# Performance work log

Hardware: AMD Instinct MI355X
Metric: run time of the kernel (lower is better)

Reference implementation:

```python
import jax, jax.numpy as jnp
import numpy as np
import math

D, S, B = 64, 2048, 16  # head_dim, seq_len, batch (inputs stored as [D, S, B])


def setup_inputs() -> dict:
    key = jax.random.key(0)
    kq, kk, kv = jax.random.split(key, 3)
    return {
        "Q": jax.random.normal(kq, (D, S, B), dtype=jnp.float32),
        "K": jax.random.normal(kk, (D, S, B), dtype=jnp.float32),
        "V": jax.random.normal(kv, (D, S, B), dtype=jnp.float32),
        "d_k": S,
    }


def reference(Q, K, V, d_k):
    # transpose(0, 2): [D, S, B] -> [B, S, D]
    q = jnp.transpose(Q, (2, 1, 0))
    k = jnp.transpose(K, (2, 1, 0))
    v = jnp.transpose(V, (2, 1, 0))
    # bmm(_Q, K_T) * 1/sqrt(d_k): [B, S, S]
    scores = jnp.einsum("bsd,btd->bst", q, k) * (1.0 / math.sqrt(d_k))
    # original does view(-1, d_k) + Softmax over dim=1; with d_k == last dim
    # this is a softmax over the key axis. Dropout is identity in eval mode.
    probs = jax.nn.softmax(scores, axis=-1)
    out = jnp.einsum("bst,btd->bsd", probs, v)  # [B, S, D]
    # transpose(0, 2) back: [D, S, B]
    return jnp.transpose(out, (2, 1, 0))
```

## Files before the change

### kernel.cpp

```cpp
#include <hip/hip_runtime.h>
#include <hip/hip_bf16.h>

#define D_ 64
#define S_ 2048
#define B_ 16
#define QT 64
#define KVT 128

typedef short short8 __attribute__((ext_vector_type(8)));
typedef float floatx4 __attribute__((ext_vector_type(4)));
typedef unsigned uint2v __attribute__((ext_vector_type(2)));
typedef unsigned uint4v __attribute__((ext_vector_type(4)));

#define SC2 (1.4426950408889634f / 45.254833995939045f)

__device__ __forceinline__ unsigned short f2bf(float f) {
  unsigned u = __builtin_bit_cast(unsigned, f);
  u += 0x7fffu + ((u >> 16) & 1u);
  return (unsigned short)(u >> 16);
}

__device__ __forceinline__ unsigned pk2(float a, float b) {
  __hip_bfloat162 h = __float22bfloat162_rn(float2{a, b});
  unsigned r;
  __builtin_memcpy(&r, &h, sizeof(r));
  return r;
}

__global__ __launch_bounds__(256) void pack_all(const float* __restrict__ Q,
                                                const float* __restrict__ K,
                                                const float* __restrict__ V,
                                                unsigned short* __restrict__ Qp,
                                                unsigned short* __restrict__ Kp,
                                                unsigned short* __restrict__ Vt) {
  __shared__ __align__(16) unsigned short tile[256][72];
  const int t = threadIdx.x;
  const int bid = blockIdx.x;
  if (bid < 256) {
    const bool isK = bid >= 128;
    const float* src = isK ? K : Q;
    unsigned short* dst = isK ? Kp : Qp;
    const float scale = isK ? SC2 : 1.0f;
    const int rb = bid & 127;
    const int s0 = rb * 16;
#pragma unroll
    for (int i = 0; i < 16; i++) {
      int j = i * 256 + t;
      int d = j >> 6;
      int sb4 = (j & 63) * 4;
      const float4 v = *(const float4*)(src + (size_t)d * (S_ * B_) + s0 * B_ + sb4);
      float vv[4] = {v.x, v.y, v.z, v.w};
#pragma unroll
      for (int k = 0; k < 4; k++) {
        int sb = sb4 + k;
        tile[(sb & 15) * 16 + (sb >> 4)][d] = f2bf(vv[k] * scale);
      }
    }
    __syncthreads();
#pragma unroll
    for (int i = 0; i < 8; i++) {
      int j = i * 256 + t;
      int r = j >> 3, c = j & 7;
      int b = r >> 4, si = r & 15;
      uint4 v = *(const uint4*)(&tile[r][c * 8]);
      *(uint4*)(dst + (((size_t)(b * 128 + rb)) << 10) + ((c >> 2) << 9) +
                (((c & 3) * 16 + si) << 3)) = v;
    }
  } else {
    const int vb = bid - 256;
    const int s0 = (vb & 31) * 64;
    const int d0 = (vb >> 5) * 16;
    const int dblk = vb >> 5;
#pragma unroll
    for (int i = 0; i < 16; i++) {
      int j = i * 256 + t;
      int dd = j >> 8;
      int sb4 = (j & 255) * 4;
      const float4 v = *(const float4*)(V + (size_t)(d0 + dd) * (S_ * B_) + s0 * B_ + sb4);
      float vv[4] = {v.x, v.y, v.z, v.w};
#pragma unroll
      for (int k = 0; k < 4; k++) {
        int sb = sb4 + k;
        tile[(sb & 15) * 16 + dd][sb >> 4] = f2bf(vv[k]);
      }
    }
    __syncthreads();
#pragma unroll
    for (int i = 0; i < 8; i++) {
      int j = i * 256 + t;
      int b = j >> 7;
      int c32r = (j >> 6) & 1;
      int l = j & 63, g = l >> 4, ln = l & 15;
      const unsigned short* row = &tile[b * 16 + ln][c32r * 32];
      uint2 u0 = *(const uint2*)(row + g * 4);
      uint2 u1 = *(const uint2*)(row + 16 + g * 4);
      int c32 = (s0 >> 5) + c32r;
      uint4 o = make_uint4(u0.x, u0.y, u1.x, u1.y);
      *(uint4*)(Vt + (((size_t)(b * 64 + c32) * 4 + dblk) << 9) + l * 8) = o;
    }
  }
}

__global__ __launch_bounds__(256, 2) void attn(const unsigned short* __restrict__ Qp,
                                               const unsigned short* __restrict__ Kp,
                                               const unsigned short* __restrict__ Vt,
                                               float* __restrict__ Ot) {
  __shared__ __align__(16) char smem_[69632 + 1024];
  float* red = (float*)smem_;
  float* lred = (float*)(smem_ + 69632);

  const int tid = threadIdx.x;
  const int w = tid >> 6, l = tid & 63, g = l >> 4, ln = l & 15;
  const int b = blockIdx.x & 15;
  const int q0 = (int)(blockIdx.x >> 4) * QT;

  const unsigned short* Qb = Qp + ((size_t)b << 17);
  const unsigned short* Kb = Kp + ((size_t)b << 17);
  const unsigned short* Vb = Vt + ((size_t)b << 17);

  const unsigned short* Qw = Qb + (((size_t)(q0 >> 4)) << 10) + l * 8;
  const unsigned short* Kw = Kb + w * 2048 + l * 8;
  const unsigned short* Vw = Vb + w * 2048 + l * 8;

  short8 qf[4][2];
#pragma unroll
  for (int nf = 0; nf < 4; nf++)
#pragma unroll
    for (int ks = 0; ks < 2; ks++)
      qf[nf][ks] = *(const short8*)(Qw + nf * 1024 + ks * 512);

  short8 kf[2][2];
#pragma unroll
  for (int mf = 0; mf < 2; mf++)
#pragma unroll
    for (int ks = 0; ks < 2; ks++)
      kf[mf][ks] = *(const short8*)(Kw + mf * 1024 + ks * 512);

  short8 vf[4];
#pragma unroll
  for (int mfd = 0; mfd < 4; mfd++)
    vf[mfd] = *(const short8*)(Vw + mfd * 512);

  const short8 ones8 = {(short)0x3F80, (short)0x3F80, (short)0x3F80, (short)0x3F80,
                        (short)0x3F80, (short)0x3F80, (short)0x3F80, (short)0x3F80};
  const floatx4 ZERO = {0.f, 0.f, 0.f, 0.f};
  floatx4 oacc[4][4];
  floatx4 dacc[4];
#pragma unroll
  for (int mfd = 0; mfd < 4; mfd++)
#pragma unroll
    for (int nf = 0; nf < 4; nf++) oacc[mfd][nf] = ZERO;
#pragma unroll
  for (int nf = 0; nf < 4; nf++) dacc[nf] = ZERO;

  for (int t = 0; t < 16; t++) {
    const int tn = ((t + 1) & 15) * 8192;

    floatx4 sacc[2][4];
    __builtin_amdgcn_s_setprio(1);
#pragma unroll
    for (int mf = 0; mf < 2; mf++)
#pragma unroll
      for (int nf = 0; nf < 4; nf++)
        sacc[mf][nf] = __builtin_amdgcn_mfma_f32_16x16x32_bf16(kf[mf][0], qf[nf][0],
                                                               ZERO, 0, 0, 0);
#pragma unroll
    for (int mf = 0; mf < 2; mf++)
#pragma unroll
      for (int nf = 0; nf < 4; nf++)
        sacc[mf][nf] = __builtin_amdgcn_mfma_f32_16x16x32_bf16(kf[mf][1], qf[nf][1],
                                                               sacc[mf][nf], 0, 0, 0);
    __builtin_amdgcn_s_setprio(0);

#pragma unroll
    for (int mf = 0; mf < 2; mf++)
#pragma unroll
      for (int ks = 0; ks < 2; ks++)
        kf[mf][ks] = *(const short8*)(Kw + tn + mf * 1024 + ks * 512);

    short8 pbf[4];
#pragma unroll
    for (int nf = 0; nf < 4; nf++) {
      unsigned p00 = pk2(__builtin_amdgcn_exp2f(sacc[0][nf][0]),
                         __builtin_amdgcn_exp2f(sacc[0][nf][1]));
      unsigned p01 = pk2(__builtin_amdgcn_exp2f(sacc[0][nf][2]),
                         __builtin_amdgcn_exp2f(sacc[0][nf][3]));
      unsigned p10 = pk2(__builtin_amdgcn_exp2f(sacc[1][nf][0]),
                         __builtin_amdgcn_exp2f(sacc[1][nf][1]));
      unsigned p11 = pk2(__builtin_amdgcn_exp2f(sacc[1][nf][2]),
                         __builtin_amdgcn_exp2f(sacc[1][nf][3]));
      pbf[nf] = __builtin_bit_cast(short8, (uint4v){p00, p01, p10, p11});
    }

    __builtin_amdgcn_s_setprio(1);
#pragma unroll
    for (int nf = 0; nf < 4; nf++)
      dacc[nf] = __builtin_amdgcn_mfma_f32_16x16x32_bf16(ones8, pbf[nf], dacc[nf], 0, 0, 0);

#pragma unroll
    for (int mfd = 0; mfd < 4; mfd++)
#pragma unroll
      for (int nf = 0; nf < 4; nf++)
        oacc[mfd][nf] = __builtin_amdgcn_mfma_f32_16x16x32_bf16(vf[mfd], pbf[nf],
                                                                oacc[mfd][nf], 0, 0, 0);
    __builtin_amdgcn_s_setprio(0);

#pragma unroll
    for (int mfd = 0; mfd < 4; mfd++)
      vf[mfd] = *(const short8*)(Vw + tn + mfd * 512);
  }

  if (g == 0) {
#pragma unroll
    for (int nf = 0; nf < 4; nf++) lred[w * 64 + nf * 16 + ln] = dacc[nf][0];
  }
#pragma unroll
  for (int mfd = 0; mfd < 4; mfd++)
#pragma unroll
    for (int nf = 0; nf < 4; nf++)
      *(floatx4*)(&red[w * 4352 + (nf * 16 + ln) * 68 + mfd * 16 + g * 4]) = oacc[mfd][nf];
  __syncthreads();

  const int q = l;
  const float denom = lred[q] + lred[64 + q] + lred[128 + q] + lred[192 + q];
  const float linv = 1.0f / denom;
#pragma unroll
  for (int i = 0; i < 4; i++) {
    floatx4 s = (floatx4){0.f, 0.f, 0.f, 0.f};
#pragma unroll
    for (int w2 = 0; w2 < 4; w2++)
      s += *(const floatx4*)(&red[w2 * 4352 + q * 68 + w * 16 + i * 4]);
    s *= linv;
#pragma unroll
    for (int r = 0; r < 4; r++)
      Ot[(size_t)(b * D_ + w * 16 + i * 4 + r) * S_ + q0 + q] = s[r];
  }
}

__global__ __launch_bounds__(256) void unpack_o(const float* __restrict__ Ot,
                                                float* __restrict__ out) {
  const int d0 = (int)(blockIdx.x & 7) * 8;
  const int s0 = (int)(blockIdx.x >> 3) * 64;
  __shared__ float u[8 * 1024];
  const int t = threadIdx.x;
#pragma unroll
  for (int i = 0; i < 8; i++) {
    int j = i * 256 + t;
    int d = j >> 8, bb = (j >> 4) & 15, c = j & 15;
    float4 v = *(const float4*)(Ot + (size_t)(bb * D_ + d0 + d) * S_ + s0 + c * 4);
    float vv[4] = {v.x, v.y, v.z, v.w};
#pragma unroll
    for (int k = 0; k < 4; k++) {
      int si = c * 4 + k;
      int W = si * 16 + bb;
      int Wp = W ^ ((si & 15) << 2);
      u[d * 1024 + Wp] = vv[k];
    }
  }
  __syncthreads();
#pragma unroll
  for (int i = 0; i < 8; i++) {
    int j = i * 256 + t;
    int d = j >> 8, c2 = j & 255;
    int G = c2 ^ ((c2 >> 2) & 15);
    float4 v = *(const float4*)(&u[d * 1024 + G * 4]);
    *(float4*)(out + (size_t)(d0 + d) * (S_ * B_) + s0 * B_ + c2 * 4) = v;
  }
}

extern "C" void kernel_launch(void* const* d_in, const int* in_sizes, int n_in,
                              void* d_out, int out_size, void* d_ws, size_t ws_size,
                              hipStream_t stream) {
  const float* Q = (const float*)d_in[0];
  const float* K = (const float*)d_in[1];
  const float* V = (const float*)d_in[2];
  float* out = (float*)d_out;
  char* ws = (char*)d_ws;
  unsigned short* Qp = (unsigned short*)(ws);
  unsigned short* Kp = (unsigned short*)(ws + (4u << 20));
  unsigned short* Vt = (unsigned short*)(ws + (8u << 20));
  float* Ot = (float*)(ws + (12u << 20));

  hipLaunchKernelGGL(pack_all, dim3(384), dim3(256), 0, stream, Q, K, V, Qp, Kp, Vt);
  hipLaunchKernelGGL(attn, dim3(512), dim3(256), 0, stream, Qp, Kp, Vt, Ot);
  hipLaunchKernelGGL(unpack_o, dim3(256), dim3(256), 0, stream, Ot, out);
}
```

Baseline: 100.8 us.

## Split query tile across wave halves and compute softmax denominators with VALU adds

The attention block grows from 256 to 512 threads. Each group of four waves now handles half the 64-query tile, so per-wave accumulators shrink and per-CU wave occupancy may rise. The row-sum MFMA against a ones vector is replaced by scalar adds of the exponentials, and the cross-wave reduction now runs in two phases through a much smaller shared buffer. Each wave still streams the same K/V, so the extra waves add more K/V load traffic per block and an extra barrier.

```diff
diff --git a/kernel.cpp b/kernel.cpp
--- a/kernel.cpp
+++ b/kernel.cpp
@@ -9,7 +9,6 @@
 
 typedef short short8 __attribute__((ext_vector_type(8)));
 typedef float floatx4 __attribute__((ext_vector_type(4)));
-typedef unsigned uint2v __attribute__((ext_vector_type(2)));
 typedef unsigned uint4v __attribute__((ext_vector_type(4)));
 
 #define SC2 (1.4426950408889634f / 45.254833995939045f)
@@ -101,16 +100,16 @@
   }
 }
 
-__global__ __launch_bounds__(256, 2) void attn(const unsigned short* __restrict__ Qp,
+__global__ __launch_bounds__(512, 4) void attn(const unsigned short* __restrict__ Qp,
                                                const unsigned short* __restrict__ Kp,
                                                const unsigned short* __restrict__ Vt,
                                                float* __restrict__ Ot) {
-  __shared__ __align__(16) char smem_[69632 + 1024];
-  float* red = (float*)smem_;
-  float* lred = (float*)(smem_ + 69632);
+  __shared__ __align__(16) float red[2][2][32][68];
+  __shared__ float lred[2][4][4][32];
 
   const int tid = threadIdx.x;
   const int w = tid >> 6, l = tid & 63, g = l >> 4, ln = l & 15;
+  const int qh = w >> 2, ksw = w & 3;
   const int b = blockIdx.x & 15;
   const int q0 = (int)(blockIdx.x >> 4) * QT;
 
@@ -118,13 +117,13 @@
   const unsigned short* Kb = Kp + ((size_t)b << 17);
   const unsigned short* Vb = Vt + ((size_t)b << 17);
 
-  const unsigned short* Qw = Qb + (((size_t)(q0 >> 4)) << 10) + l * 8;
-  const unsigned short* Kw = Kb + w * 2048 + l * 8;
-  const unsigned short* Vw = Vb + w * 2048 + l * 8;
-
-  short8 qf[4][2];
-#pragma unroll
-  for (int nf = 0; nf < 4; nf++)
+  const unsigned short* Qw = Qb + (((size_t)((q0 >> 4) + qh * 2)) << 10) + l * 8;
+  const unsigned short* Kw = Kb + ksw * 2048 + l * 8;
+  const unsigned short* Vw = Vb + ksw * 2048 + l * 8;
+
+  short8 qf[2][2];
+#pragma unroll
+  for (int nf = 0; nf < 2; nf++)
 #pragma unroll
     for (int ks = 0; ks < 2; ks++)
       qf[nf][ks] = *(const short8*)(Qw + nf * 1024 + ks * 512);
@@ -141,33 +140,29 @@
   for (int mfd = 0; mfd < 4; mfd++)
     vf[mfd] = *(const short8*)(Vw + mfd * 512);
 
-  const short8 ones8 = {(short)0x3F80, (short)0x3F80, (short)0x3F80, (short)0x3F80,
-                        (short)0x3F80, (short)0x3F80, (short)0x3F80, (short)0x3F80};
   const floatx4 ZERO = {0.f, 0.f, 0.f, 0.f};
-  floatx4 oacc[4][4];
-  floatx4 dacc[4];
+  floatx4 oacc[4][2];
+  float dacc[2] = {0.f, 0.f};
 #pragma unroll
   for (int mfd = 0; mfd < 4; mfd++)
 #pragma unroll
-    for (int nf = 0; nf < 4; nf++) oacc[mfd][nf] = ZERO;
-#pragma unroll
-  for (int nf = 0; nf < 4; nf++) dacc[nf] = ZERO;
+    for (int nf = 0; nf < 2; nf++) oacc[mfd][nf] = ZERO;
 
   for (int t = 0; t < 16; t++) {
     const int tn = ((t + 1) & 15) * 8192;
 
-    floatx4 sacc[2][4];
+    floatx4 sacc[2][2];
     __builtin_amdgcn_s_setprio(1);
 #pragma unroll
     for (int mf = 0; mf < 2; mf++)
 #pragma unroll
-      for (int nf = 0; nf < 4; nf++)
+      for (int nf = 0; nf < 2; nf++)
         sacc[mf][nf] = __builtin_amdgcn_mfma_f32_16x16x32_bf16(kf[mf][0], qf[nf][0],
                                                                ZERO, 0, 0, 0);
 #pragma unroll
     for (int mf = 0; mf < 2; mf++)
 #pragma unroll
-      for (int nf = 0; nf < 4; nf++)
+      for (int nf = 0; nf < 2; nf++)
         sacc[mf][nf] = __builtin_amdgcn_mfma_f32_16x16x32_bf16(kf[mf][1], qf[nf][1],
                                                                sacc[mf][nf], 0, 0, 0);
     __builtin_amdgcn_s_setprio(0);
@@ -178,29 +173,28 @@
       for (int ks = 0; ks < 2; ks++)
         kf[mf][ks] = *(const short8*)(Kw + tn + mf * 1024 + ks * 512);
 
-    short8 pbf[4];
-#pragma unroll
-    for (int nf = 0; nf < 4; nf++) {
-      unsigned p00 = pk2(__builtin_amdgcn_exp2f(sacc[0][nf][0]),
-                         __builtin_amdgcn_exp2f(sacc[0][nf][1]));
-      unsigned p01 = pk2(__builtin_amdgcn_exp2f(sacc[0][nf][2]),
-                         __builtin_amdgcn_exp2f(sacc[0][nf][3]));
-      unsigned p10 = pk2(__builtin_amdgcn_exp2f(sacc[1][nf][0]),
-                         __builtin_amdgcn_exp2f(sacc[1][nf][1]));
-      unsigned p11 = pk2(__builtin_amdgcn_exp2f(sacc[1][nf][2]),
-                         __builtin_amdgcn_exp2f(sacc[1][nf][3]));
+    short8 pbf[2];
+#pragma unroll
+    for (int nf = 0; nf < 2; nf++) {
+      float e0 = __builtin_amdgcn_exp2f(sacc[0][nf][0]);
+      float e1 = __builtin_amdgcn_exp2f(sacc[0][nf][1]);
+      float e2 = __builtin_amdgcn_exp2f(sacc[0][nf][2]);
+      float e3 = __builtin_amdgcn_exp2f(sacc[0][nf][3]);
+      float e4 = __builtin_amdgcn_exp2f(sacc[1][nf][0]);
+      float e5 = __builtin_amdgcn_exp2f(sacc[1][nf][1]);
+      float e6 = __builtin_amdgcn_exp2f(sacc[1][nf][2]);
+      float e7 = __builtin_amdgcn_exp2f(sacc[1][nf][3]);
+      unsigned p00 = pk2(e0, e1), p01 = pk2(e2, e3);
+      unsigned p10 = pk2(e4, e5), p11 = pk2(e6, e7);
       pbf[nf] = __builtin_bit_cast(short8, (uint4v){p00, p01, p10, p11});
+      dacc[nf] += ((e0 + e1) + (e2 + e3)) + ((e4 + e5) + (e6 + e7));
     }
 
     __builtin_amdgcn_s_setprio(1);
 #pragma unroll
-    for (int nf = 0; nf < 4; nf++)
-      dacc[nf] = __builtin_amdgcn_mfma_f32_16x16x32_bf16(ones8, pbf[nf], dacc[nf], 0, 0, 0);
-
-#pragma unroll
-    for (int mfd = 0; mfd < 4; mfd++)
-#pragma unroll
-      for (int nf = 0; nf < 4; nf++)
+    for (int mfd = 0; mfd < 4; mfd++)
+#pragma unroll
+      for (int nf = 0; nf < 2; nf++)
         oacc[mfd][nf] = __builtin_amdgcn_mfma_f32_16x16x32_bf16(vf[mfd], pbf[nf],
                                                                 oacc[mfd][nf], 0, 0, 0);
     __builtin_amdgcn_s_setprio(0);
@@ -210,30 +204,47 @@
       vf[mfd] = *(const short8*)(Vw + tn + mfd * 512);
   }
 
-  if (g == 0) {
-#pragma unroll
-    for (int nf = 0; nf < 4; nf++) lred[w * 64 + nf * 16 + ln] = dacc[nf][0];
-  }
-#pragma unroll
-  for (int mfd = 0; mfd < 4; mfd++)
-#pragma unroll
-    for (int nf = 0; nf < 4; nf++)
-      *(floatx4*)(&red[w * 4352 + (nf * 16 + ln) * 68 + mfd * 16 + g * 4]) = oacc[mfd][nf];
+#pragma unroll
+  for (int nf = 0; nf < 2; nf++)
+    lred[qh][ksw][g][nf * 16 + ln] = dacc[nf];
+  if (ksw < 2) {
+#pragma unroll
+    for (int mfd = 0; mfd < 4; mfd++)
+#pragma unroll
+      for (int nf = 0; nf < 2; nf++)
+        *(floatx4*)(&red[qh][ksw][nf * 16 + ln][mfd * 16 + g * 4]) = oacc[mfd][nf];
+  }
   __syncthreads();
-
-  const int q = l;
-  const float denom = lred[q] + lred[64 + q] + lred[128 + q] + lred[192 + q];
+  if (ksw >= 2) {
+#pragma unroll
+    for (int mfd = 0; mfd < 4; mfd++)
+#pragma unroll
+      for (int nf = 0; nf < 2; nf++) {
+        float* p = &red[qh][ksw - 2][nf * 16 + ln][mfd * 16 + g * 4];
+        *(floatx4*)p = *(const floatx4*)p + oacc[mfd][nf];
+      }
+  }
+  __syncthreads();
+
+  const int q = l & 31;
+  const int dh = (l >> 5) * 8;
+  float denom = 0.f;
+#pragma unroll
+  for (int kk = 0; kk < 4; kk++)
+#pragma unroll
+    for (int gg = 0; gg < 4; gg++) denom += lred[qh][kk][gg][q];
   const float linv = 1.0f / denom;
-#pragma unroll
-  for (int i = 0; i < 4; i++) {
-    floatx4 s = (floatx4){0.f, 0.f, 0.f, 0.f};
-#pragma unroll
-    for (int w2 = 0; w2 < 4; w2++)
-      s += *(const floatx4*)(&red[w2 * 4352 + q * 68 + w * 16 + i * 4]);
+  const int dq = ksw;
+  const int qcol = q0 + qh * 32 + q;
+#pragma unroll
+  for (int i = 0; i < 2; i++) {
+    const int d = dq * 16 + dh + i * 4;
+    floatx4 s = *(const floatx4*)(&red[qh][0][q][d]) +
+                *(const floatx4*)(&red[qh][1][q][d]);
     s *= linv;
 #pragma unroll
     for (int r = 0; r < 4; r++)
-      Ot[(size_t)(b * D_ + w * 16 + i * 4 + r) * S_ + q0 + q] = s[r];
+      Ot[(size_t)(b * D_ + d + r) * S_ + qcol] = s[r];
   }
 }
 
@@ -282,6 +293,6 @@
   float* Ot = (float*)(ws + (12u << 20));
 
   hipLaunchKernelGGL(pack_all, dim3(384), dim3(256), 0, stream, Q, K, V, Qp, Kp, Vt);
-  hipLaunchKernelGGL(attn, dim3(512), dim3(256), 0, stream, Qp, Kp, Vt, Ot);
+  hipLaunchKernelGGL(attn, dim3(512), dim3(512), 0, stream, Qp, Kp, Vt, Ot);
   hipLaunchKernelGGL(unpack_o, dim3(256), dim3(256), 0, stream, Ot, out);
 }
```

Result: slower. 106.5 us (+5.6%).

## Software-pipeline QK^T scores one tile ahead with ping-pong accumulators

Applied to the files above, without the earlier changes.

Restructures the KV loop so the QK^T MFMAs for the next tile are issued before the exp2/pack and PV MFMAs of the current tile, using two ping-pong score buffers and a manually unrolled by-two loop. K fragments are now prefetched two tiles ahead. The aim is to overlap the transcendental/VALU softmax work with matrix-core work from independent tiles. It raises VGPR pressure with an extra 8 floatx4 accumulators, which may lower occupancy or cause spills. The final iteration computes an extra wrapped-around score tile that is discarded.

```diff
diff --git a/kernel.cpp b/kernel.cpp
--- a/kernel.cpp
+++ b/kernel.cpp
@@ -9,7 +9,6 @@
 
 typedef short short8 __attribute__((ext_vector_type(8)));
 typedef float floatx4 __attribute__((ext_vector_type(4)));
-typedef unsigned uint2v __attribute__((ext_vector_type(2)));
 typedef unsigned uint4v __attribute__((ext_vector_type(4)));
 
 #define SC2 (1.4426950408889634f / 45.254833995939045f)
@@ -153,42 +152,65 @@
 #pragma unroll
   for (int nf = 0; nf < 4; nf++) dacc[nf] = ZERO;
 
-  for (int t = 0; t < 16; t++) {
-    const int tn = ((t + 1) & 15) * 8192;
-
-    floatx4 sacc[2][4];
+  floatx4 sA[2][4], sB[2][4];
+
+  __builtin_amdgcn_s_setprio(1);
+#pragma unroll
+  for (int mf = 0; mf < 2; mf++)
+#pragma unroll
+    for (int nf = 0; nf < 4; nf++)
+      sA[mf][nf] = __builtin_amdgcn_mfma_f32_16x16x32_bf16(kf[mf][0], qf[nf][0],
+                                                           ZERO, 0, 0, 0);
+#pragma unroll
+  for (int mf = 0; mf < 2; mf++)
+#pragma unroll
+    for (int nf = 0; nf < 4; nf++)
+      sA[mf][nf] = __builtin_amdgcn_mfma_f32_16x16x32_bf16(kf[mf][1], qf[nf][1],
+                                                           sA[mf][nf], 0, 0, 0);
+  __builtin_amdgcn_s_setprio(0);
+#pragma unroll
+  for (int mf = 0; mf < 2; mf++)
+#pragma unroll
+    for (int ks = 0; ks < 2; ks++)
+      kf[mf][ks] = *(const short8*)(Kw + 8192 + mf * 1024 + ks * 512);
+
+  auto step = [&](floatx4 (&cur)[2][4], floatx4 (&nxt)[2][4], int t)
+      __attribute__((always_inline)) {
+    const int tn1 = ((t + 1) & 15) * 8192;
+    const int tn2 = ((t + 2) & 15) * 8192;
+
     __builtin_amdgcn_s_setprio(1);
 #pragma unroll
     for (int mf = 0; mf < 2; mf++)
 #pragma unroll
       for (int nf = 0; nf < 4; nf++)
-        sacc[mf][nf] = __builtin_amdgcn_mfma_f32_16x16x32_bf16(kf[mf][0], qf[nf][0],
-                                                               ZERO, 0, 0, 0);
+        nxt[mf][nf] = __builtin_amdgcn_mfma_f32_16x16x32_bf16(kf[mf][0], qf[nf][0],
+                                                              ZERO, 0, 0, 0);
 #pragma unroll
     for (int mf = 0; mf < 2; mf++)
 #pragma unroll
       for (int nf = 0; nf < 4; nf++)
-        sacc[mf][nf] = __builtin_amdgcn_mfma_f32_16x16x32_bf16(kf[mf][1], qf[nf][1],
-                                                               sacc[mf][nf], 0, 0, 0);
+        nxt[mf][nf] = __builtin_amdgcn_mfma_f32_16x16x32_bf16(kf[mf][1], qf[nf][1],
+                                                              nxt[mf][nf], 0, 0, 0);
     __builtin_amdgcn_s_setprio(0);
 
 #pragma unroll
     for (int mf = 0; mf < 2; mf++)
 #pragma unroll
       for (int ks = 0; ks < 2; ks++)
-        kf[mf][ks] = *(const short8*)(Kw + tn + mf * 1024 + ks * 512);
+        kf[mf][ks] = *(const short8*)(Kw + tn2 + mf * 1024 + ks * 512);
 
     short8 pbf[4];
 #pragma unroll
     for (int nf = 0; nf < 4; nf++) {
-      unsigned p00 = pk2(__builtin_amdgcn_exp2f(sacc[0][nf][0]),
-                         __builtin_amdgcn_exp2f(sacc[0][nf][1]));
-      unsigned p01 = pk2(__builtin_amdgcn_exp2f(sacc[0][nf][2]),
-                         __builtin_amdgcn_exp2f(sacc[0][nf][3]));
-      unsigned p10 = pk2(__builtin_amdgcn_exp2f(sacc[1][nf][0]),
-                         __builtin_amdgcn_exp2f(sacc[1][nf][1]));
-      unsigned p11 = pk2(__builtin_amdgcn_exp2f(sacc[1][nf][2]),
-                         __builtin_amdgcn_exp2f(sacc[1][nf][3]));
+      unsigned p00 = pk2(__builtin_amdgcn_exp2f(cur[0][nf][0]),
+                         __builtin_amdgcn_exp2f(cur[0][nf][1]));
+      unsigned p01 = pk2(__builtin_amdgcn_exp2f(cur[0][nf][2]),
+                         __builtin_amdgcn_exp2f(cur[0][nf][3]));
+      unsigned p10 = pk2(__builtin_amdgcn_exp2f(cur[1][nf][0]),
+                         __builtin_amdgcn_exp2f(cur[1][nf][1]));
+      unsigned p11 = pk2(__builtin_amdgcn_exp2f(cur[1][nf][2]),
+                         __builtin_amdgcn_exp2f(cur[1][nf][3]));
       pbf[nf] = __builtin_bit_cast(short8, (uint4v){p00, p01, p10, p11});
     }
 
@@ -207,7 +229,13 @@
 
 #pragma unroll
     for (int mfd = 0; mfd < 4; mfd++)
-      vf[mfd] = *(const short8*)(Vw + tn + mfd * 512);
+      vf[mfd] = *(const short8*)(Vw + tn1 + mfd * 512);
+  };
+
+#pragma unroll 1
+  for (int t = 0; t < 16; t += 2) {
+    step(sA, sB, t);
+    step(sB, sA, t + 1);
   }
 
   if (g == 0) {
```

Measured after the change: 101.6 us. No clear change (+0.8%).
